# Performance work log

Hardware: AMD Instinct MI355X
Metric: run time of the kernel (lower is better)

The kernel has to match this reference:

```python
import jax, jax.numpy as jnp
import numpy as np

T, N = 24, 2048
INPUT_DIM, HIDDEN, MEDIATE, SOCIAL, OUT_DIM = 2, 64, 128, 64, 2
N_SIZE = 2
CELL = 0.3
T_OBS, T_PRED = 9, 19
WIN = (N_SIZE + 1) ** 2  # (N_size+1)^2 = 9 window cells


def _social_pool(h, coords, mask):
    """Faithful social pooling for N_size=2, grid_cell_size=0.3.

    torch builds a dynamic grid, scatter-adds every agent's h into its cell,
    then gathers grid[int(x-R):int(x+R), int(y-R):int(y+R)] per agent.
    With R=0.3 and integer positions >= 4 (guaranteed by the margin), that
    slice is exactly the single cell (x-1, y-1), broadcast over the 3x3
    window. We compute it as a pairwise match without materializing a grid.
    Runs under torch.no_grad() -> stop_gradient.
    """
    margin = 2 * N_SIZE * CELL
    lt = jnp.stack([coords[:, 0].min(), coords[:, 1].min()]) - margin
    p = jnp.floor((coords - lt) / CELL).astype(jnp.int32)            # [N,2]
    p = p * mask.astype(jnp.int32)[:, None]                          # masked agents -> cell (0,0)
    q = p - 1                                                        # gathered cell per agent
    match = (p[None, :, 0] == q[:, None, 0]) & (p[None, :, 1] == q[:, None, 1])  # [i,j]
    cell_val = match.astype(h.dtype) @ h                             # [N,hidden] scatter-add + gather
    Hf = jnp.tile(cell_val, (1, WIN)) * mask[:, None]                # broadcast over 3x3 window, flat
    return jax.lax.stop_gradient(Hf)


def _forward(X, part_masks, all_h_t, all_c_t, Y, W_in, b_in, W_soc, b_soc,
             W_ih, W_hh, b_ih, b_hh, W_out, b_out, T_obs, T_pred):
    relu = jax.nn.relu  # dropout_prob = 0 -> Phi == ReLU

    def lstm(z, h, c):
        g = z @ W_ih.T + b_ih + h @ W_hh.T + b_hh
        i, f, gg, o = jnp.split(g, 4, axis=1)
        c = jax.nn.sigmoid(f) * c + jax.nn.sigmoid(i) * jnp.tanh(gg)
        h = jax.nn.sigmoid(o) * jnp.tanh(c)
        return h, c

    def cell_out(r, h, c, coords, m):
        Hf = _social_pool(h, coords, m)
        e = relu(Hf @ W_soc.T + b_soc)
        z = jnp.concatenate([r, e], axis=1)
        h, c = lstm(z, h, c)
        out = (h @ W_out.T + b_out) * m[:, None]
        return h, c, out

    def step_obs(carry, inp):
        h, c = carry
        x, m = inp
        r = relu(x @ W_in.T + b_in)
        h, c, out = cell_out(r, h, c, x, m)
        return (h, c), out

    (h, c), outs_obs = jax.lax.scan(
        step_obs, (all_h_t, all_c_t), (X[:T_obs + 1], part_masks[:T_obs + 1]))

    def step_pred(carry, inp):
        h, c, last_pt, prev_out = carry
        x, m = inp
        r = relu(last_pt @ W_in.T + b_in)
        h, c, out = cell_out(r, h, c, x, m)
        # torch: last_point = outputs[frame_idx - 1] AFTER the frame runs
        return (h, c, prev_out, out), out

    carry0 = (h, c, X[T_obs + 1], outs_obs[-1])
    _, outs_pred = jax.lax.scan(
        step_pred, carry0, (X[T_obs + 1:T_pred + 1], part_masks[T_obs + 1:T_pred + 1]))

    tail = jnp.zeros((X.shape[0] - T_pred - 1, X.shape[1], OUT_DIM), X.dtype)
    return jnp.concatenate([outs_obs, outs_pred, tail], axis=0)


def setup_inputs() -> dict:
    key = jax.random.key(0)
    ks = jax.random.split(key, 13)

    def lin(kw, kb, out_d, in_d):  # torch nn.Linear default init
        lim = 1.0 / float(np.sqrt(in_d))
        W = jax.random.uniform(kw, (out_d, in_d), minval=-lim, maxval=lim, dtype=jnp.float32)
        b = jax.random.uniform(kb, (out_d,), minval=-lim, maxval=lim, dtype=jnp.float32)
        return W, b

    W_in, b_in = lin(ks[0], ks[1], MEDIATE, INPUT_DIM)
    W_soc, b_soc = lin(ks[2], ks[3], SOCIAL, WIN * HIDDEN)
    W_ih, b_ih = lin(ks[4], ks[5], 4 * HIDDEN, MEDIATE + SOCIAL)
    W_hh, b_hh = lin(ks[6], ks[7], 4 * HIDDEN, HIDDEN)
    W_out, b_out = lin(ks[8], ks[9], OUT_DIM, HIDDEN)

    X = jax.random.normal(ks[10], (T, N, INPUT_DIM), dtype=jnp.float32) * 10.0  # meter-scale coords
    part_masks = (jax.random.uniform(ks[11], (T, N)) < 0.9).astype(jnp.float32)  # binary presence mask
    Y = jax.random.normal(ks[12], (T, N, INPUT_DIM), dtype=jnp.float32)  # unused by forward
    all_h_t = jnp.zeros((N, HIDDEN), jnp.float32)
    all_c_t = jnp.zeros((N, HIDDEN), jnp.float32)

    return {"X": X, "part_masks": part_masks, "all_h_t": all_h_t, "all_c_t": all_c_t,
            "Y": Y, "T_obs": T_OBS, "T_pred": T_PRED,
            "W_in": W_in, "b_in": b_in, "W_soc": W_soc, "b_soc": b_soc,
            "W_ih": W_ih, "W_hh": W_hh, "b_ih": b_ih, "b_hh": b_hh,
            "W_out": W_out, "b_out": b_out}


def reference(X, part_masks, all_h_t, all_c_t, Y, T_obs, T_pred,
              W_in, b_in, W_soc, b_soc, W_ih, W_hh, b_ih, b_hh, W_out, b_out):
    return _forward(X, part_masks, all_h_t, all_c_t, Y, W_in, b_in, W_soc, b_soc,
                    W_ih, W_hh, b_ih, b_hh, W_out, b_out, int(T_obs), int(T_pred))
```

## Files before the change

### kernel.cpp

```cpp
#include <hip/hip_runtime.h>
#include <math.h>


#define N_AG   2048
#define STEPS  20
#define CAP    12
#define NSRV   21
#define MAGIC  0x13572468

typedef short short8 __attribute__((ext_vector_type(8)));
typedef float f32x4  __attribute__((ext_vector_type(4)));
union FU { uint4 q; short8 v; };

__device__ __forceinline__ unsigned short bf16rne(float x) {
    unsigned u = __float_as_uint(x);
    unsigned r = (u + 0x7fff + ((u >> 16) & 1)) >> 16;
    return (unsigned short)r;
}

__device__ __forceinline__ int khash(int k) {
    return (int)(((unsigned)k * 2654435761u) >> 21);
}

__device__ __forceinline__ float fsigm(float x) {
    return __builtin_amdgcn_rcpf(1.f + __expf(-x));
}
__device__ __forceinline__ float ftanh(float x) {
    float e = __expf(2.f * x);
    return 1.f - 2.f * __builtin_amdgcn_rcpf(e + 1.f);
}

__device__ __forceinline__ void bar_lds() {
    asm volatile("s_waitcnt lgkmcnt(0)\n\ts_barrier" ::: "memory");
}

__device__ __forceinline__ void ast(int* p_, int v) {
    __hip_atomic_store(p_, v, __ATOMIC_RELAXED, __HIP_MEMORY_SCOPE_AGENT);
}
__device__ __forceinline__ void astf(float* p_, float v) {
    __hip_atomic_store(p_, v, __ATOMIC_RELAXED, __HIP_MEMORY_SCOPE_AGENT);
}

struct KP {
    const float *X, *masks, *h_in, *c_in;
    const float *Win, *bin, *Wsoc, *bsoc, *Wih, *Whh, *bih, *bhh, *Wout, *bout;
    float *Wef;
    int *mcnt, *midx, *need, *flags;
    float *out;
    unsigned long long *hist;
};

__global__ __launch_bounds__(512, 1) void k_all(KP p)
{
    __shared__ __align__(16) uint4 zshq[544];
    __shared__ __align__(16) uint4 zslq[544];
    __shared__ float gbuf[16][258];
    __shared__ float cvs[16][64];
    __shared__ float hs[16][68];
    __shared__ float sWefP[64 * 65];
    __shared__ float2 sWinP[16 * 17];
    __shared__ float sBinP[16 * 9];
    __shared__ float sX[11][16][2];
    __shared__ float sMask[STEPS][16];
    __shared__ int   sCnt[STEPS][16];
    __shared__ int   sNeed[19][16];
    __shared__ int   sMidx[STEPS][16][CAP];
    __shared__ float sBsoc[64], sBc[256], sWout[128], sBout[2];
    __shared__ uint4 sE0h[8], sE0l[8];
    __shared__ float olocal[2][16][2];
    __shared__ int kk[N_AG];
    __shared__ int head[N_AG];
    __shared__ int nxt[N_AG];
    __shared__ float red[512];

    const int tid = threadIdx.x;
    const int bxg = blockIdx.x;

    if (bxg < NSRV) {
        const int sb = bxg;
        {
            int lo = sb * 780;
            int hi = (sb == NSRV - 1) ? 16384 : lo + 780;
            for (int i = lo + tid; i < hi; i += 512)
                p.out[20 * N_AG * 2 + i] = 0.f;
        }
        if (sb == 20) {
            for (int i = tid; i < 4096; i += 512) {
                int s = i >> 6, k = i & 63;
                float a = 0.f;
                #pragma unroll
                for (int w = 0; w < 9; w++) a += p.Wsoc[s * 576 + w * 64 + k];
                astf(&p.Wef[i], a);
            }
            __syncthreads();
            if (tid == 0) ast(&p.flags[20], MAGIC);
            return;
        }

        const int t = sb;
        const float* Xt = p.X + t * N_AG * 2;

        float mnx = 1e30f, mny = 1e30f;
        for (int i = tid; i < N_AG; i += 512) {
            mnx = fminf(mnx, Xt[2 * i]);
            mny = fminf(mny, Xt[2 * i + 1]);
        }
        red[tid] = mnx; __syncthreads();
        for (int s = 256; s > 0; s >>= 1) { if (tid < s) red[tid] = fminf(red[tid], red[tid + s]); __syncthreads(); }
        float ltx = red[0]; __syncthreads();
        red[tid] = mny; __syncthreads();
        for (int s = 256; s > 0; s >>= 1) { if (tid < s) red[tid] = fminf(red[tid], red[tid + s]); __syncthreads(); }
        float lty = red[0]; __syncthreads();
        ltx -= 1.2f;
        lty -= 1.2f;

        for (int i = tid; i < N_AG; i += 512) {
            float m = p.masks[t * N_AG + i];
            int px = (int)floorf((Xt[2 * i]     - ltx) / 0.3f);
            int py = (int)floorf((Xt[2 * i + 1] - lty) / 0.3f);
            int im = (int)m;
            px *= im; py *= im;
            kk[i] = px * 65536 + py;
            head[i] = -1;
            if (t >= 1) ast(&p.need[(t - 1) * N_AG + i], 0);
        }
        __syncthreads();
        for (int j = tid; j < N_AG; j += 512) {
            int kj = kk[j];
            if (kj != 0) nxt[j] = atomicExch(&head[khash(kj)], j);
        }
        __syncthreads();
        for (int i = tid; i < N_AG; i += 512) {
            int ki = kk[i];
            int cnt = 0;
            int base = (t * N_AG + i) * CAP;
            if (ki != 0) {
                int tkey = ki - 65537;
                int lst[CAP];
                for (int j = head[khash(tkey)]; j >= 0; j = nxt[j]) {
                    if (kk[j] == tkey) { if (cnt < CAP) lst[cnt] = j; cnt++; }
                }
                if (cnt > CAP) cnt = CAP;
                for (int a = 1; a < cnt; a++) {
                    int v = lst[a]; int b = a - 1;
                    while (b >= 0 && lst[b] > v) { lst[b + 1] = lst[b]; b--; }
                    lst[b + 1] = v;
                }
                for (int a = 0; a < cnt; a++) {
                    ast(&p.midx[base + a], lst[a]);
                    if (t >= 1) ast(&p.need[(t - 1) * N_AG + lst[a]], 1);
                }
            }
            ast(&p.mcnt[t * N_AG + i], cnt);
        }
        __syncthreads();
        if (tid == 0) ast(&p.flags[t], MAGIC);
        return;
    }

    const int bx    = bxg - NSRV;
    const int wbase = bx * 16;
    const int wv    = tid >> 6, lane = tid & 63;
    const int mA    = lane & 15, quad = lane >> 4;
    const int nt0   = 2 * wv;

    if (tid < 256) sBc[tid] = p.bih[tid] + p.bhh[tid];
    if (tid < 128) {
        sWout[tid] = p.Wout[tid];
        int c = tid;
        sWinP[(c >> 3) * 17 + (c & 7)] = make_float2(p.Win[2 * c], p.Win[2 * c + 1]);
        sBinP[(c >> 3) * 9 + (c & 7)] = p.bin[c];
    }
    if (tid < 64) sBsoc[tid] = p.bsoc[tid];
    if (tid < 2)  sBout[tid] = p.bout[tid];
    if (tid < 8) {
        unsigned uh[4], ul[4];
        #pragma unroll
        for (int w = 0; w < 4; w++) {
            float v0 = fmaxf(p.bsoc[tid * 8 + 2 * w], 0.f);
            float v1 = fmaxf(p.bsoc[tid * 8 + 2 * w + 1], 0.f);
            unsigned short h0 = bf16rne(v0), h1 = bf16rne(v1);
            float f0 = __uint_as_float(((unsigned)h0) << 16);
            float f1 = __uint_as_float(((unsigned)h1) << 16);
            unsigned short l0 = bf16rne(v0 - f0), l1 = bf16rne(v1 - f1);
            uh[w] = (unsigned)h0 | ((unsigned)h1 << 16);
            ul[w] = (unsigned)l0 | ((unsigned)l1 << 16);
        }
        sE0h[tid] = make_uint4(uh[0], uh[1], uh[2], uh[3]);
        sE0l[tid] = make_uint4(ul[0], ul[1], ul[2], ul[3]);
    }
    if (tid < 352) { int tt = tid / 32, r = tid % 32;
                     sX[tt][r >> 1][r & 1] = p.X[tt * (N_AG * 2) + (wbase + (r >> 1)) * 2 + (r & 1)]; }
    if (tid < 320) { int tt = tid / 16, m2 = tid % 16;
                     sMask[tt][m2] = p.masks[tt * N_AG + wbase + m2]; }

    float c0, c1;
    {
        int m0 = tid >> 6, h0i = tid & 63, m1 = m0 + 8;
        hs[m0][h0i] = p.h_in[(wbase + m0) * 64 + h0i];
        hs[m1][h0i] = p.h_in[(wbase + m1) * 64 + h0i];
        c0 = p.c_in[(wbase + m0) * 64 + h0i];
        c1 = p.c_in[(wbase + m1) * 64 + h0i];
    }

    FU wh[2][8], wl[2][8];
    #pragma unroll
    for (int e = 0; e < 2; e++) {
        int g = (nt0 + e) * 16 + mA;
        #pragma unroll
        for (int kt = 0; kt < 8; kt++) {
            int k0 = kt * 32 + quad * 8;
            const float* src = (k0 < 192) ? (p.Wih + g * 192 + k0)
                                          : (p.Whh + g * 64 + (k0 - 192));
            unsigned uh[4], ul[4];
            #pragma unroll
            for (int w = 0; w < 4; w++) {
                float a = src[2 * w], b = src[2 * w + 1];
                unsigned short ha = bf16rne(a), hb = bf16rne(b);
                float fa = __uint_as_float(((unsigned)ha) << 16);
                float fb = __uint_as_float(((unsigned)hb) << 16);
                unsigned short la = bf16rne(a - fa), lb = bf16rne(b - fb);
                uh[w] = (unsigned)ha | ((unsigned)hb << 16);
                ul[w] = (unsigned)la | ((unsigned)lb << 16);
            }
            wh[e][kt].q = make_uint4(uh[0], uh[1], uh[2], uh[3]);
            wl[e][kt].q = make_uint4(ul[0], ul[1], ul[2], ul[3]);
        }
    }

    if (tid < NSRV) {
        while (__hip_atomic_load(&p.flags[tid], __ATOMIC_RELAXED,
                                 __HIP_MEMORY_SCOPE_AGENT) != MAGIC) { }
    }
    __syncthreads();

    if (tid < 320) { int tt = tid / 16, m2 = tid % 16;
                     sCnt[tt][m2] = p.mcnt[tt * N_AG + wbase + m2]; }
    if (tid < 304) { int s = tid / 16, m2 = tid % 16;
                     sNeed[s][m2] = p.need[s * N_AG + wbase + m2]; }
    for (int i = tid; i < 4096; i += 512) sWefP[(i >> 6) * 65 + (i & 63)] = p.Wef[i];
    for (int i = tid; i < STEPS * 16 * CAP; i += 512) {
        int tt = i / (16 * CAP), r = i % (16 * CAP), m2 = r / CAP, n = r % CAP;
        sMidx[tt][m2][n] = p.midx[(tt * N_AG + wbase + m2) * CAP + n];
    }
    __syncthreads();

    #pragma unroll 1
    for (int t = 0; t < STEPS; t++) {
        const int m5 = tid >> 5, s5 = tid & 31;
        const int cnt5 = sCnt[t][m5];

        {
            if (s5 < 16) {
                float px, py;
                if (t <= 10) { px = sX[t][m5][0];         py = sX[t][m5][1]; }
                else         { px = olocal[t & 1][m5][0]; py = olocal[t & 1][m5][1]; }
                float v[8];
                #pragma unroll
                for (int j = 0; j < 8; j++) {
                    float2 w2 = sWinP[s5 * 17 + j];
                    v[j] = fmaxf(w2.x * px + w2.y * py + sBinP[s5 * 9 + j], 0.f);
                }
                unsigned uh[4], ul[4];
                #pragma unroll
                for (int w = 0; w < 4; w++) {
                    float v0 = v[2 * w], v1 = v[2 * w + 1];
                    unsigned short h0 = bf16rne(v0), h1 = bf16rne(v1);
                    float f0 = __uint_as_float(((unsigned)h0) << 16);
                    float f1 = __uint_as_float(((unsigned)h1) << 16);
                    unsigned short l0 = bf16rne(v0 - f0), l1 = bf16rne(v1 - f1);
                    uh[w] = (unsigned)h0 | ((unsigned)h1 << 16);
                    ul[w] = (unsigned)l0 | ((unsigned)l1 << 16);
                }
                zshq[s5 * 17 + m5] = make_uint4(uh[0], uh[1], uh[2], uh[3]);
                zslq[s5 * 17 + m5] = make_uint4(ul[0], ul[1], ul[2], ul[3]);
            } else if (s5 < 24) {
                if (cnt5 == 0) {
                    zshq[s5 * 17 + m5] = sE0h[s5 - 16];
                    zslq[s5 * 17 + m5] = sE0l[s5 - 16];
                }
            } else {
                float v[8];
                #pragma unroll
                for (int j = 0; j < 8; j++) v[j] = hs[m5][(s5 - 24) * 8 + j];
                unsigned uh[4], ul[4];
                #pragma unroll
                for (int w = 0; w < 4; w++) {
                    float v0 = v[2 * w], v1 = v[2 * w + 1];
                    unsigned short h0 = bf16rne(v0), h1 = bf16rne(v1);
                    float f0 = __uint_as_float(((unsigned)h0) << 16);
                    float f1 = __uint_as_float(((unsigned)h1) << 16);
                    unsigned short l0 = bf16rne(v0 - f0), l1 = bf16rne(v1 - f1);
                    uh[w] = (unsigned)h0 | ((unsigned)h1 << 16);
                    ul[w] = (unsigned)l0 | ((unsigned)l1 << 16);
                }
                zshq[s5 * 17 + m5] = make_uint4(uh[0], uh[1], uh[2], uh[3]);
                zslq[s5 * 17 + m5] = make_uint4(ul[0], ul[1], ul[2], ul[3]);
            }
        }
        bar_lds();

        if (cnt5 > 0) {
            float a0 = 0.f, a1 = 0.f;
            if (t == 0) {
                for (int n = 0; n < cnt5; n++) {
                    int r = sMidx[0][m5][n];
                    a0 += p.h_in[r * 64 + s5];
                    a1 += p.h_in[r * 64 + s5 + 32];
                }
            } else {
                const unsigned long long* hb = p.hist + (size_t)(t - 1) * (N_AG * 64);
                const unsigned tagw = (unsigned)t;
                for (int n = 0; n < cnt5; n++) {
                    int r = sMidx[t][m5][n];
                    unsigned long long w0, w1;
                    do {
                        w0 = __hip_atomic_load(&hb[r * 64 + s5], __ATOMIC_RELAXED,
                                               __HIP_MEMORY_SCOPE_AGENT);
                        w1 = __hip_atomic_load(&hb[r * 64 + s5 + 32], __ATOMIC_RELAXED,
                                               __HIP_MEMORY_SCOPE_AGENT);
                    } while ((unsigned)(w0 >> 32) != tagw || (unsigned)(w1 >> 32) != tagw);
                    a0 += __uint_as_float((unsigned)w0);
                    a1 += __uint_as_float((unsigned)w1);
                }
            }
            cvs[m5][s5] = a0; cvs[m5][s5 + 32] = a1;
            float acc0 = sBsoc[s5], acc1 = sBsoc[s5 + 32];
            const float* w0p = &sWefP[s5 * 65];
            const float* w1p = &sWefP[(s5 + 32) * 65];
            for (int k = 0; k < 64; k++) {
                float cv = cvs[m5][k];
                acc0 += cv * w0p[k];
                acc1 += cv * w1p[k];
            }
            acc0 = fmaxf(acc0, 0.f);
            acc1 = fmaxf(acc1, 0.f);
            const int base = (m5 & 1) * 32;
            float v[8];
            #pragma unroll
            for (int jj = 0; jj < 8; jj++) {
                int c = s5 * 8 + jj;
                int srcl = base + ((c < 32 ? c : c - 32) & 31);
                float va = __shfl(acc0, srcl, 64);
                float vb = __shfl(acc1, srcl, 64);
                v[jj] = (c < 32) ? va : vb;
            }
            if (s5 < 8) {
                unsigned uh[4], ul[4];
                #pragma unroll
                for (int w = 0; w < 4; w++) {
                    float v0 = v[2 * w], v1 = v[2 * w + 1];
                    unsigned short h0 = bf16rne(v0), h1 = bf16rne(v1);
                    float f0 = __uint_as_float(((unsigned)h0) << 16);
                    float f1 = __uint_as_float(((unsigned)h1) << 16);
                    unsigned short l0 = bf16rne(v0 - f0), l1 = bf16rne(v1 - f1);
                    uh[w] = (unsigned)h0 | ((unsigned)h1 << 16);
                    ul[w] = (unsigned)l0 | ((unsigned)l1 << 16);
                }
                zshq[(16 + s5) * 17 + m5] = make_uint4(uh[0], uh[1], uh[2], uh[3]);
                zslq[(16 + s5) * 17 + m5] = make_uint4(ul[0], ul[1], ul[2], ul[3]);
            }
        }

        f32x4 a0v = {0.f, 0.f, 0.f, 0.f};
        f32x4 a1v = {0.f, 0.f, 0.f, 0.f};
        #pragma unroll
        for (int u = 0; u < 6; u++) {
            const int kt = (u < 4) ? u : u + 2;
            int fi = (kt * 4 + quad) * 17 + mA;
            FU az, bz;
            az.q = zshq[fi];
            bz.q = zslq[fi];
            a0v = __builtin_amdgcn_mfma_f32_16x16x32_bf16(az.v, wh[0][kt].v, a0v, 0, 0, 0);
            a1v = __builtin_amdgcn_mfma_f32_16x16x32_bf16(az.v, wh[1][kt].v, a1v, 0, 0, 0);
            a0v = __builtin_amdgcn_mfma_f32_16x16x32_bf16(bz.v, wh[0][kt].v, a0v, 0, 0, 0);
            a1v = __builtin_amdgcn_mfma_f32_16x16x32_bf16(bz.v, wh[1][kt].v, a1v, 0, 0, 0);
            a0v = __builtin_amdgcn_mfma_f32_16x16x32_bf16(az.v, wl[0][kt].v, a0v, 0, 0, 0);
            a1v = __builtin_amdgcn_mfma_f32_16x16x32_bf16(az.v, wl[1][kt].v, a1v, 0, 0, 0);
        }
        bar_lds();

        #pragma unroll
        for (int kt = 4; kt <= 5; kt++) {
            int fi = (kt * 4 + quad) * 17 + mA;
            FU az, bz;
            az.q = zshq[fi];
            bz.q = zslq[fi];
            a0v = __builtin_amdgcn_mfma_f32_16x16x32_bf16(az.v, wh[0][kt].v, a0v, 0, 0, 0);
            a1v = __builtin_amdgcn_mfma_f32_16x16x32_bf16(az.v, wh[1][kt].v, a1v, 0, 0, 0);
            a0v = __builtin_amdgcn_mfma_f32_16x16x32_bf16(bz.v, wh[0][kt].v, a0v, 0, 0, 0);
            a1v = __builtin_amdgcn_mfma_f32_16x16x32_bf16(bz.v, wh[1][kt].v, a1v, 0, 0, 0);
            a0v = __builtin_amdgcn_mfma_f32_16x16x32_bf16(az.v, wl[0][kt].v, a0v, 0, 0, 0);
            a1v = __builtin_amdgcn_mfma_f32_16x16x32_bf16(az.v, wl[1][kt].v, a1v, 0, 0, 0);
        }
        #pragma unroll
        for (int r = 0; r < 4; r++) {
            int row = quad * 4 + r;
            gbuf[row][nt0 * 16 + mA]       = a0v[r];
            gbuf[row][(nt0 + 1) * 16 + mA] = a1v[r];
        }
        bar_lds();

        {
            int m0 = tid >> 6, hid = tid & 63, m1 = m0 + 8;
            float hn0, hn1;
            {
                float gi = gbuf[m0][hid]       + sBc[hid];
                float gf = gbuf[m0][64 + hid]  + sBc[64 + hid];
                float gR = gbuf[m0][128 + hid] + sBc[128 + hid];
                float go = gbuf[m0][192 + hid] + sBc[192 + hid];
                float cn = fsigm(gf) * c0 + fsigm(gi) * ftanh(gR);
                hn0 = fsigm(go) * ftanh(cn);
                c0 = cn;
                hs[m0][hid] = hn0;
            }
            {
                float gi = gbuf[m1][hid]       + sBc[hid];
                float gf = gbuf[m1][64 + hid]  + sBc[64 + hid];
                float gR = gbuf[m1][128 + hid] + sBc[128 + hid];
                float go = gbuf[m1][192 + hid] + sBc[192 + hid];
                float cn = fsigm(gf) * c1 + fsigm(gi) * ftanh(gR);
                hn1 = fsigm(go) * ftanh(cn);
                c1 = cn;
                hs[m1][hid] = hn1;
            }
            if (t <= 18) {
                unsigned long long* hp = p.hist + (size_t)t * (N_AG * 64);
                unsigned long long tg = ((unsigned long long)(t + 1)) << 32;
                if (sNeed[t][m0])
                    __hip_atomic_store(&hp[(wbase + m0) * 64 + hid],
                                       tg | (unsigned long long)__float_as_uint(hn0),
                                       __ATOMIC_RELAXED, __HIP_MEMORY_SCOPE_AGENT);
                if (sNeed[t][m1])
                    __hip_atomic_store(&hp[(wbase + m1) * 64 + hid],
                                       tg | (unsigned long long)__float_as_uint(hn1),
                                       __ATOMIC_RELAXED, __HIP_MEMORY_SCOPE_AGENT);
            }

            float w0 = sWout[hid], w1 = sWout[64 + hid];
            float p00 = hn0 * w0, p01 = hn0 * w1;
            float p10 = hn1 * w0, p11 = hn1 * w1;
            #pragma unroll
            for (int off = 32; off >= 1; off >>= 1) {
                p00 += __shfl_xor(p00, off);
                p01 += __shfl_xor(p01, off);
                p10 += __shfl_xor(p10, off);
                p11 += __shfl_xor(p11, off);
            }
            if (hid == 0) {
                float mk0 = sMask[t][m0], mk1 = sMask[t][m1];
                float o00 = (p00 + sBout[0]) * mk0, o01 = (p01 + sBout[1]) * mk0;
                float o10 = (p10 + sBout[0]) * mk1, o11 = (p11 + sBout[1]) * mk1;
                p.out[(t * N_AG + wbase + m0) * 2 + 0] = o00;
                p.out[(t * N_AG + wbase + m0) * 2 + 1] = o01;
                p.out[(t * N_AG + wbase + m1) * 2 + 0] = o10;
                p.out[(t * N_AG + wbase + m1) * 2 + 1] = o11;
                olocal[t & 1][m0][0] = o00; olocal[t & 1][m0][1] = o01;
                olocal[t & 1][m1][0] = o10; olocal[t & 1][m1][1] = o11;
            }
        }
        bar_lds();
    }
}

extern "C" void kernel_launch(void* const* d_in, const int* in_sizes, int n_in,
                              void* d_out, int out_size, void* d_ws, size_t ws_size,
                              hipStream_t stream)
{
    KP kp;
    kp.X     = (const float*)d_in[0];
    kp.masks = (const float*)d_in[1];
    kp.h_in  = (const float*)d_in[2];
    kp.c_in  = (const float*)d_in[3];
    kp.Win   = (const float*)d_in[7];
    kp.bin   = (const float*)d_in[8];
    kp.Wsoc  = (const float*)d_in[9];
    kp.bsoc  = (const float*)d_in[10];
    kp.Wih   = (const float*)d_in[11];
    kp.Whh   = (const float*)d_in[12];
    kp.bih   = (const float*)d_in[13];
    kp.bhh   = (const float*)d_in[14];
    kp.Wout  = (const float*)d_in[15];
    kp.bout  = (const float*)d_in[16];
    kp.out   = (float*)d_out;

    unsigned long long* hist = (unsigned long long*)d_ws;
    float* Wef  = (float*)(hist + 19 * N_AG * 64);
    int*   need = (int*)(Wef + 4096);
    int*   mcnt = need + 19 * N_AG;
    int*   midx = mcnt + STEPS * N_AG;
    int*   flags = midx + STEPS * N_AG * CAP;

    kp.hist = hist; kp.Wef = Wef; kp.need = need; kp.mcnt = mcnt;
    kp.midx = midx; kp.flags = flags;

    k_all<<<NSRV + 128, 512, 0, stream>>>(kp);
}
```

Baseline: 190.0 us.

## Stream per-step neighbor tables lazily and read local agents' hidden state from LDS

The upfront wait on all precompute flags is replaced by per-step flag waits. Each step's mcnt, need and midx rows are loaded at the end of the previous step, so the recurrent loop can start before every server block has finished. Neighbor gathers now read hidden state from the block's own shared hs buffer when the neighbor belongs to the same block, skipping global spin-loads. Neighbors are also processed in pairs so two remote loads are in flight together. This adds correctness risk: hs must hold the matching previous-step values, and flag dependencies are split across many waits.

```diff
diff --git a/kernel.cpp b/kernel.cpp
--- a/kernel.cpp
+++ b/kernel.cpp
@@ -39,6 +39,12 @@
 }
 __device__ __forceinline__ void astf(float* p_, float v) {
     __hip_atomic_store(p_, v, __ATOMIC_RELAXED, __HIP_MEMORY_SCOPE_AGENT);
+}
+__device__ __forceinline__ int ald(const int* p_) {
+    return __hip_atomic_load(p_, __ATOMIC_RELAXED, __HIP_MEMORY_SCOPE_AGENT);
+}
+__device__ __forceinline__ void spinflag(const int* f_) {
+    while (ald(f_) != MAGIC) { }
 }
 
 struct KP {
@@ -228,20 +234,19 @@
         }
     }
 
-    if (tid < NSRV) {
-        while (__hip_atomic_load(&p.flags[tid], __ATOMIC_RELAXED,
-                                 __HIP_MEMORY_SCOPE_AGENT) != MAGIC) { }
-    }
-    __syncthreads();
-
-    if (tid < 320) { int tt = tid / 16, m2 = tid % 16;
-                     sCnt[tt][m2] = p.mcnt[tt * N_AG + wbase + m2]; }
-    if (tid < 304) { int s = tid / 16, m2 = tid % 16;
-                     sNeed[s][m2] = p.need[s * N_AG + wbase + m2]; }
-    for (int i = tid; i < 4096; i += 512) sWefP[(i >> 6) * 65 + (i & 63)] = p.Wef[i];
-    for (int i = tid; i < STEPS * 16 * CAP; i += 512) {
-        int tt = i / (16 * CAP), r = i % (16 * CAP), m2 = r / CAP, n = r % CAP;
-        sMidx[tt][m2][n] = p.midx[(tt * N_AG + wbase + m2) * CAP + n];
+    if (tid < 16) { spinflag(&p.flags[0]);
+                    sCnt[0][tid] = ald(&p.mcnt[0 * N_AG + wbase + tid]); }
+    else if (tid < 32) { spinflag(&p.flags[1]);
+                    sNeed[0][tid - 16] = ald(&p.need[0 * N_AG + wbase + (tid - 16)]); }
+    else if (tid >= 64 && tid < 64 + 192) {
+        spinflag(&p.flags[0]);
+        int q = tid - 64; int m2 = q / CAP, n = q % CAP;
+        sMidx[0][m2][n] = ald(&p.midx[(0 * N_AG + wbase + m2) * CAP + n]);
+    }
+    {
+        spinflag(&p.flags[20]);
+        for (int i = tid; i < 4096; i += 512)
+            sWefP[(i >> 6) * 65 + (i & 63)] = p.Wef[i];
     }
     __syncthreads();
 
@@ -311,17 +316,51 @@
             } else {
                 const unsigned long long* hb = p.hist + (size_t)(t - 1) * (N_AG * 64);
                 const unsigned tagw = (unsigned)t;
-                for (int n = 0; n < cnt5; n++) {
+                int n = 0;
+                while (n + 1 < cnt5) {
+                    int r0 = sMidx[t][m5][n], r1 = sMidx[t][m5][n + 1];
+                    bool in0 = (unsigned)(r0 - wbase) < 16u;
+                    bool in1 = (unsigned)(r1 - wbase) < 16u;
+                    float b00, b01, b10, b11;
+                    if (in0) { b00 = hs[r0 - wbase][s5]; b01 = hs[r0 - wbase][s5 + 32]; }
+                    if (in1) { b10 = hs[r1 - wbase][s5]; b11 = hs[r1 - wbase][s5 + 32]; }
+                    if (!in0 || !in1) {
+                        unsigned long long w00, w01, w10, w11;
+                        bool bad;
+                        do {
+                            bad = false;
+                            if (!in0) {
+                                w00 = __hip_atomic_load(&hb[r0 * 64 + s5], __ATOMIC_RELAXED, __HIP_MEMORY_SCOPE_AGENT);
+                                w01 = __hip_atomic_load(&hb[r0 * 64 + s5 + 32], __ATOMIC_RELAXED, __HIP_MEMORY_SCOPE_AGENT);
+                                bad |= ((unsigned)(w00 >> 32) != tagw) | ((unsigned)(w01 >> 32) != tagw);
+                            }
+                            if (!in1) {
+                                w10 = __hip_atomic_load(&hb[r1 * 64 + s5], __ATOMIC_RELAXED, __HIP_MEMORY_SCOPE_AGENT);
+                                w11 = __hip_atomic_load(&hb[r1 * 64 + s5 + 32], __ATOMIC_RELAXED, __HIP_MEMORY_SCOPE_AGENT);
+                                bad |= ((unsigned)(w10 >> 32) != tagw) | ((unsigned)(w11 >> 32) != tagw);
+                            }
+                        } while (bad);
+                        if (!in0) { b00 = __uint_as_float((unsigned)w00); b01 = __uint_as_float((unsigned)w01); }
+                        if (!in1) { b10 = __uint_as_float((unsigned)w10); b11 = __uint_as_float((unsigned)w11); }
+                    }
+                    a0 += b00; a1 += b01;
+                    a0 += b10; a1 += b11;
+                    n += 2;
+                }
+                if (n < cnt5) {
                     int r = sMidx[t][m5][n];
-                    unsigned long long w0, w1;
-                    do {
-                        w0 = __hip_atomic_load(&hb[r * 64 + s5], __ATOMIC_RELAXED,
-                                               __HIP_MEMORY_SCOPE_AGENT);
-                        w1 = __hip_atomic_load(&hb[r * 64 + s5 + 32], __ATOMIC_RELAXED,
-                                               __HIP_MEMORY_SCOPE_AGENT);
-                    } while ((unsigned)(w0 >> 32) != tagw || (unsigned)(w1 >> 32) != tagw);
-                    a0 += __uint_as_float((unsigned)w0);
-                    a1 += __uint_as_float((unsigned)w1);
+                    if ((unsigned)(r - wbase) < 16u) {
+                        a0 += hs[r - wbase][s5];
+                        a1 += hs[r - wbase][s5 + 32];
+                    } else {
+                        unsigned long long w0, w1;
+                        do {
+                            w0 = __hip_atomic_load(&hb[r * 64 + s5], __ATOMIC_RELAXED, __HIP_MEMORY_SCOPE_AGENT);
+                            w1 = __hip_atomic_load(&hb[r * 64 + s5 + 32], __ATOMIC_RELAXED, __HIP_MEMORY_SCOPE_AGENT);
+                        } while ((unsigned)(w0 >> 32) != tagw || (unsigned)(w1 >> 32) != tagw);
+                        a0 += __uint_as_float((unsigned)w0);
+                        a1 += __uint_as_float((unsigned)w1);
+                    }
                 }
             }
             cvs[m5][s5] = a0; cvs[m5][s5 + 32] = a1;
@@ -457,6 +496,21 @@
                 p.out[(t * N_AG + wbase + m1) * 2 + 1] = o11;
                 olocal[t & 1][m0][0] = o00; olocal[t & 1][m0][1] = o01;
                 olocal[t & 1][m1][0] = o10; olocal[t & 1][m1][1] = o11;
+            }
+
+            if (t < STEPS - 1) {
+                const int tn = t + 1;
+                if (tid < 16) {
+                    spinflag(&p.flags[tn]);
+                    sCnt[tn][tid] = ald(&p.mcnt[tn * N_AG + wbase + tid]);
+                } else if (tid < 32 && tn <= 18) {
+                    spinflag(&p.flags[tn + 1]);
+                    sNeed[tn][tid - 16] = ald(&p.need[tn * N_AG + wbase + (tid - 16)]);
+                } else if (tid >= 64 && tid < 64 + 192) {
+                    spinflag(&p.flags[tn]);
+                    int q = tid - 64; int m2 = q / CAP, n = q % CAP;
+                    sMidx[tn][m2][n] = ald(&p.midx[(tn * N_AG + wbase + m2) * CAP + n]);
+                }
             }
         }
         bar_lds();
```

Result: slower. 196.2 us (+3.3%).
